# Optimization experiments

Hardware: AMD Instinct MI355X
Metric: run time of the kernel (lower is better)

Reference implementation:

```python
import jax, jax.numpy as jnp
import numpy as np

B, S, D = 8, 512, 768
H, C = 256, 32


def setup_inputs() -> dict:
    key = jax.random.key(0)
    ks = jax.random.split(key, 8)
    scale = 0.05
    return {
        "seq_feats": jax.random.normal(ks[0], (B, S, D), jnp.float32),
        "U": jax.random.normal(ks[1], (H, C, H), jnp.float32) * scale,
        "W_w": jax.random.normal(ks[2], (C, 2 * H), jnp.float32) * scale,
        "W_b": jax.random.normal(ks[3], (C,), jnp.float32) * scale,
        "Ws_w": jax.random.normal(ks[4], (H, D), jnp.float32) * scale,
        "Ws_b": jax.random.normal(ks[5], (H,), jnp.float32) * scale,
        "We_w": jax.random.normal(ks[6], (H, D), jnp.float32) * scale,
        "We_b": jax.random.normal(ks[7], (H,), jnp.float32) * scale,
    }


def reference(seq_feats, U, W_w, W_b, Ws_w, Ws_b, We_w, We_b):
    # start / end projections (torch Linear: x @ W.T + b)
    Hs = seq_feats @ Ws_w.T + Ws_b  # [B,S,H]
    He = seq_feats @ We_w.T + We_b  # [B,S,H]
    # bilinear term: h_s^T U h_e per label
    biaff = jnp.einsum('bsh,hcg,beg->bsec', Hs, U, He)  # [B,S,S,C]
    # concat-linear term rewritten as two broadcast matmuls:
    # W([Hs;He]) = Hs @ W_s.T + He @ W_e.T + b  (identical math, no [B,S,S,2H] intermediate)
    h = Hs.shape[-1]
    W_s, W_e = W_w[:, :h], W_w[:, h:]
    lin = (Hs @ W_s.T)[:, :, None, :] + (He @ W_e.T)[:, None, :, :] + W_b
    return biaff + lin
```

## Files before the change

### kernel.cpp

```cpp
#include <hip/hip_runtime.h>


typedef __bf16 bf16x8 __attribute__((ext_vector_type(8)));
typedef float f32x4 __attribute__((ext_vector_type(4)));
typedef unsigned int u32x4 __attribute__((ext_vector_type(4)));
typedef unsigned int u32x2 __attribute__((ext_vector_type(2)));

union BF8 { unsigned short s[8]; unsigned int u[4]; bf16x8 v; };

__device__ __forceinline__ unsigned short f2bf(float f) {
    unsigned u = __builtin_bit_cast(unsigned, f);
    u += 0x7fffu + ((u >> 16) & 1u);
    return (unsigned short)(u >> 16);
}
__device__ __forceinline__ float bf2f(unsigned short s) {
    unsigned u = ((unsigned)s) << 16;
    return __builtin_bit_cast(float, u);
}
__device__ __forceinline__ bf16x8 load_bf8(const unsigned short* p) {
    return __builtin_bit_cast(bf16x8, *reinterpret_cast<const uint4*>(p));
}
__device__ __forceinline__ ushort4 pack4(float4 v) {
    ushort4 r;
    r.x = f2bf(v.x); r.y = f2bf(v.y); r.z = f2bf(v.z); r.w = f2bf(v.w);
    return r;
}

__global__ __launch_bounds__(256) void kp_conv(
    const float* __restrict__ seq, const float* __restrict__ Ws_w,
    const float* __restrict__ We_w, unsigned short* __restrict__ seqb,
    unsigned short* __restrict__ Wcat) {
    int i = blockIdx.x * 256 + threadIdx.x;
    if (i < 786432) {
        float4 v = ((const float4*)seq)[i];
        ((ushort4*)seqb)[i] = pack4(v);
    } else {
        int j = i - 786432;
        float4 v = (j < 49152) ? ((const float4*)Ws_w)[j]
                               : ((const float4*)We_w)[j - 49152];
        ((ushort4*)Wcat)[j] = pack4(v);
    }
}

__global__ __launch_bounds__(256) void k0_ut(const float* __restrict__ U,
                                             unsigned short* __restrict__ Ut) {
    __shared__ float tile[32][33];
    int tx = threadIdx.x, ty = threadIdx.y;
    int J0 = blockIdx.x * 32, h0 = blockIdx.y * 32;
#pragma unroll
    for (int i = 0; i < 4; i++)
        tile[ty + 8 * i][tx] = U[(h0 + ty + 8 * i) * 8192 + J0 + tx];
    __syncthreads();
#pragma unroll
    for (int i = 0; i < 4; i++)
        Ut[(J0 + ty + 8 * i) * 256 + h0 + tx] = f2bf(tile[tx][ty + 8 * i]);
}

__global__ __launch_bounds__(256) void k1_hs_he(
    const unsigned short* __restrict__ seqb, const unsigned short* __restrict__ Wcat,
    const float* __restrict__ Ws_b, const float* __restrict__ We_b,
    unsigned short* __restrict__ Hs, unsigned short* __restrict__ He) {
    int wid = threadIdx.x >> 6, lane = threadIdx.x & 63;
    int t = lane & 15, q = lane >> 4;
    int wave_id = blockIdx.x * 4 + wid;
    int m0 = (wave_id >> 4) * 32;
    int n0 = (wave_id & 15) * 32;

    const unsigned short* a0 = seqb + (size_t)(m0 + t) * 768;
    const unsigned short* a1 = seqb + (size_t)(m0 + 16 + t) * 768;
    const unsigned short* b0 = Wcat + (size_t)(n0 + t) * 768;
    const unsigned short* b1 = Wcat + (size_t)(n0 + 16 + t) * 768;

    f32x4 acc[2][2];
#pragma unroll
    for (int i = 0; i < 2; i++)
#pragma unroll
        for (int j = 0; j < 2; j++) acc[i][j] = {0.f, 0.f, 0.f, 0.f};

#pragma unroll 4
    for (int kk = 0; kk < 24; kk++) {
        int k = kk * 32 + q * 8;
        bf16x8 af0 = load_bf8(a0 + k);
        bf16x8 af1 = load_bf8(a1 + k);
        bf16x8 bf0 = load_bf8(b0 + k);
        bf16x8 bf1 = load_bf8(b1 + k);
        acc[0][0] = __builtin_amdgcn_mfma_f32_16x16x32_bf16(af0, bf0, acc[0][0], 0, 0, 0);
        acc[0][1] = __builtin_amdgcn_mfma_f32_16x16x32_bf16(af0, bf1, acc[0][1], 0, 0, 0);
        acc[1][0] = __builtin_amdgcn_mfma_f32_16x16x32_bf16(af1, bf0, acc[1][0], 0, 0, 0);
        acc[1][1] = __builtin_amdgcn_mfma_f32_16x16x32_bf16(af1, bf1, acc[1][1], 0, 0, 0);
    }
#pragma unroll
    for (int nt = 0; nt < 2; nt++) {
        int col = n0 + nt * 16 + t;
        float bv;
        unsigned short* dst;
        int c2;
        if (col < 256) { bv = Ws_b[col]; dst = Hs; c2 = col; }
        else           { bv = We_b[col - 256]; dst = He; c2 = col - 256; }
#pragma unroll
        for (int mt = 0; mt < 2; mt++)
#pragma unroll
            for (int r = 0; r < 4; r++) {
                int row = m0 + mt * 16 + q * 4 + r;
                dst[row * 256 + c2] = f2bf(acc[mt][nt][r] + bv);
            }
    }
}

__global__ __launch_bounds__(256) void k2_lin(
    const unsigned short* __restrict__ Hs, const float* __restrict__ W_w,
    const float* __restrict__ W_b, float* __restrict__ linS) {
    int idx = blockIdx.x * 256 + threadIdx.x;
    int c = idx & 31;
    int bs = idx >> 5;
    const unsigned short* Hrow = Hs + bs * 256;
    const float* Wrow = W_w + c * 512;
    float acc = W_b[c];
#pragma unroll 4
    for (int h8 = 0; h8 < 32; h8++) {
        BF8 hv;
        hv.v = load_bf8(Hrow + h8 * 8);
        float4 w0 = *(const float4*)(Wrow + h8 * 8);
        float4 w1 = *(const float4*)(Wrow + h8 * 8 + 4);
        acc += bf2f(hv.s[0]) * w0.x + bf2f(hv.s[1]) * w0.y + bf2f(hv.s[2]) * w0.z +
               bf2f(hv.s[3]) * w0.w + bf2f(hv.s[4]) * w1.x + bf2f(hv.s[5]) * w1.y +
               bf2f(hv.s[6]) * w1.z + bf2f(hv.s[7]) * w1.w;
    }
    linS[bs * 32 + c] = acc;
}

__global__ __launch_bounds__(256) void k3_T(
    const unsigned short* __restrict__ Hs, const unsigned short* __restrict__ Ut,
    const float* __restrict__ W_w, unsigned short* __restrict__ T) {
    int wid = threadIdx.x >> 6, lane = threadIdx.x & 63;
    int t = lane & 15, q = lane >> 4;
    int n_blk = blockIdx.x & 63;
    int mb = (blockIdx.x >> 6) * 4 + wid;
    int c = n_blk >> 1;
    int g0 = (n_blk & 1) * 128;
    int s0 = mb * 32;

    bf16x8 hfr[2][8];
#pragma unroll
    for (int mt = 0; mt < 2; mt++) {
        const unsigned short* arow = Hs + (size_t)(s0 + mt * 16 + t) * 256 + q * 8;
#pragma unroll
        for (int kk = 0; kk < 8; kk++) hfr[mt][kk] = load_bf8(arow + kk * 32);
    }
#pragma unroll 2
    for (int nt = 0; nt < 8; nt++) {
        const unsigned short* grow = Ut + (size_t)(c * 256 + g0 + nt * 16 + t) * 256 + q * 8;
        float4 we = *(const float4*)(W_w + c * 512 + 256 + g0 + nt * 16 + q * 4);
        f32x4 acc0 = {we.x, we.y, we.z, we.w};
        f32x4 acc1 = acc0;
#pragma unroll
        for (int kk = 0; kk < 8; kk++) {
            bf16x8 g = load_bf8(grow + kk * 32);
            acc0 = __builtin_amdgcn_mfma_f32_16x16x32_bf16(g, hfr[0][kk], acc0, 0, 0, 0);
            acc1 = __builtin_amdgcn_mfma_f32_16x16x32_bf16(g, hfr[1][kk], acc1, 0, 0, 0);
        }
        int gidx = g0 + nt * 16 + q * 4;
        u32x2 p0, p1;
        p0.x = (unsigned)f2bf(acc0[0]) | ((unsigned)f2bf(acc0[1]) << 16);
        p0.y = (unsigned)f2bf(acc0[2]) | ((unsigned)f2bf(acc0[3]) << 16);
        p1.x = (unsigned)f2bf(acc1[0]) | ((unsigned)f2bf(acc1[1]) << 16);
        p1.y = (unsigned)f2bf(acc1[2]) | ((unsigned)f2bf(acc1[3]) << 16);
        __builtin_nontemporal_store(p0, (u32x2*)(T + (size_t)((s0 + t) * 32 + c) * 256 + gidx));
        __builtin_nontemporal_store(p1, (u32x2*)(T + (size_t)((s0 + 16 + t) * 32 + c) * 256 + gidx));
    }
}

__global__ __launch_bounds__(256) void k4_out(
    const unsigned short* __restrict__ T, const unsigned short* __restrict__ He,
    const float* __restrict__ linS, float* __restrict__ out) {
    int wid = threadIdx.x >> 6, lane = threadIdx.x & 63;
    int t = lane & 15, q = lane >> 4;
    int b = blockIdx.x & 7;
    int s = (blockIdx.x >> 3) * 4 + wid;
    int bs = b * 512 + s;

    bf16x8 tfr[2][8];
#pragma unroll
    for (int ct = 0; ct < 2; ct++) {
        const unsigned short* brow = T + (size_t)(bs * 32 + ct * 16 + t) * 256 + q * 8;
#pragma unroll
        for (int kk = 0; kk < 8; kk++) {
            u32x4 r = __builtin_nontemporal_load((const u32x4*)(brow + kk * 32));
            tfr[ct][kk] = __builtin_bit_cast(bf16x8, r);
        }
    }
    f32x4 ls0, ls1;
    {
        float4 a = *(const float4*)(linS + bs * 32 + q * 4);
        float4 bv = *(const float4*)(linS + bs * 32 + 16 + q * 4);
        ls0 = {a.x, a.y, a.z, a.w};
        ls1 = {bv.x, bv.y, bv.z, bv.w};
    }
    float* orow = out + (size_t)bs * (512 * 32);
#pragma unroll 2
    for (int e_t = 0; e_t < 32; e_t++) {
        int e0 = e_t * 16;
        const unsigned short* arow = He + (size_t)(b * 512 + e0 + t) * 256 + q * 8;
        f32x4 acc0 = ls0, acc1 = ls1;
#pragma unroll
        for (int kk = 0; kk < 8; kk++) {
            bf16x8 a = load_bf8(arow + kk * 32);
            acc0 = __builtin_amdgcn_mfma_f32_16x16x32_bf16(tfr[0][kk], a, acc0, 0, 0, 0);
            acc1 = __builtin_amdgcn_mfma_f32_16x16x32_bf16(tfr[1][kk], a, acc1, 0, 0, 0);
        }
        float* p = orow + (size_t)(e0 + t) * 32 + q * 4;
        __builtin_nontemporal_store(acc0, (f32x4*)p);
        __builtin_nontemporal_store(acc1, (f32x4*)(p + 16));
    }
}

extern "C" void kernel_launch(void* const* d_in, const int* in_sizes, int n_in,
                              void* d_out, int out_size, void* d_ws, size_t ws_size,
                              hipStream_t stream) {
    const float* seq  = (const float*)d_in[0];
    const float* U    = (const float*)d_in[1];
    const float* W_w  = (const float*)d_in[2];
    const float* W_b  = (const float*)d_in[3];
    const float* Ws_w = (const float*)d_in[4];
    const float* Ws_b = (const float*)d_in[5];
    const float* We_w = (const float*)d_in[6];
    const float* We_b = (const float*)d_in[7];
    float* out = (float*)d_out;

    char* ws = (char*)d_ws;
    unsigned short* Hs   = (unsigned short*)(ws);
    unsigned short* He   = (unsigned short*)(ws + (2ull << 20));
    unsigned short* Ut   = (unsigned short*)(ws + (4ull << 20));
    float* linS          = (float*)(ws + (8ull << 20));
    unsigned short* seqb = (unsigned short*)(ws + (9ull << 20));
    unsigned short* Wcat = (unsigned short*)(ws + (15ull << 20));
    unsigned short* T    = (unsigned short*)(ws + (16ull << 20));

    kp_conv<<<3456, 256, 0, stream>>>(seq, Ws_w, We_w, seqb, Wcat);
    k0_ut<<<dim3(256, 8), dim3(32, 8), 0, stream>>>(U, Ut);
    k1_hs_he<<<512, 256, 0, stream>>>(seqb, Wcat, Ws_b, We_b, Hs, He);
    k2_lin<<<512, 256, 0, stream>>>(Hs, W_w, W_b, linS);
    k3_T<<<2048, 256, 0, stream>>>(Hs, Ut, W_w, T);
    k4_out<<<1024, 256, 0, stream>>>(T, He, linS, out);
}
```

Baseline: 509.2 us.

## Enlarge per-wave register tiles and double-buffer operand loads in k3 and k4

k3_T now covers 64 rows of Hs per wave instead of 32, and k4_out covers two s rows per wave. Each loaded Ut or He fragment therefore feeds twice as many MFMAs, and both grids are halved to match. The next tile's B-operand fragments are prefetched into an alternate register buffer while the current tile's MFMAs run, to hide global load latency. The cost is much higher VGPR use, which may lower occupancy. k4's prefetch also reads one tile past the end of He on the last iteration; the values are never used.

```diff
diff --git a/kernel.cpp b/kernel.cpp
--- a/kernel.cpp
+++ b/kernel.cpp
@@ -138,36 +138,55 @@
     int mb = (blockIdx.x >> 6) * 4 + wid;
     int c = n_blk >> 1;
     int g0 = (n_blk & 1) * 128;
-    int s0 = mb * 32;
-
-    bf16x8 hfr[2][8];
-#pragma unroll
-    for (int mt = 0; mt < 2; mt++) {
+    int s0 = mb * 64;
+
+    bf16x8 hfr[4][8];
+#pragma unroll
+    for (int mt = 0; mt < 4; mt++) {
         const unsigned short* arow = Hs + (size_t)(s0 + mt * 16 + t) * 256 + q * 8;
 #pragma unroll
         for (int kk = 0; kk < 8; kk++) hfr[mt][kk] = load_bf8(arow + kk * 32);
     }
-#pragma unroll 2
-    for (int nt = 0; nt < 8; nt++) {
-        const unsigned short* grow = Ut + (size_t)(c * 256 + g0 + nt * 16 + t) * 256 + q * 8;
-        float4 we = *(const float4*)(W_w + c * 512 + 256 + g0 + nt * 16 + q * 4);
-        f32x4 acc0 = {we.x, we.y, we.z, we.w};
-        f32x4 acc1 = acc0;
-#pragma unroll
-        for (int kk = 0; kk < 8; kk++) {
-            bf16x8 g = load_bf8(grow + kk * 32);
-            acc0 = __builtin_amdgcn_mfma_f32_16x16x32_bf16(g, hfr[0][kk], acc0, 0, 0, 0);
-            acc1 = __builtin_amdgcn_mfma_f32_16x16x32_bf16(g, hfr[1][kk], acc1, 0, 0, 0);
-        }
-        int gidx = g0 + nt * 16 + q * 4;
-        u32x2 p0, p1;
-        p0.x = (unsigned)f2bf(acc0[0]) | ((unsigned)f2bf(acc0[1]) << 16);
-        p0.y = (unsigned)f2bf(acc0[2]) | ((unsigned)f2bf(acc0[3]) << 16);
-        p1.x = (unsigned)f2bf(acc1[0]) | ((unsigned)f2bf(acc1[1]) << 16);
-        p1.y = (unsigned)f2bf(acc1[2]) | ((unsigned)f2bf(acc1[3]) << 16);
-        __builtin_nontemporal_store(p0, (u32x2*)(T + (size_t)((s0 + t) * 32 + c) * 256 + gidx));
-        __builtin_nontemporal_store(p1, (u32x2*)(T + (size_t)((s0 + 16 + t) * 32 + c) * 256 + gidx));
-    }
+
+    const unsigned short* gbase = Ut + (size_t)(c * 256 + g0 + t) * 256 + q * 8;
+    bf16x8 g_cur[8], g_alt[8];
+#pragma unroll
+    for (int kk = 0; kk < 8; kk++) g_cur[kk] = load_bf8(gbase + kk * 32);
+
+#define K3_BODY(NT, GC, GN)                                                      \
+    {                                                                            \
+        const int nt = (NT);                                                     \
+        if (nt + 1 < 8) {                                                        \
+            const unsigned short* gn = gbase + (size_t)(nt + 1) * 16 * 256;      \
+            _Pragma("unroll") for (int kk = 0; kk < 8; kk++)                     \
+                GN[kk] = load_bf8(gn + kk * 32);                                 \
+        }                                                                        \
+        float4 we = *(const float4*)(W_w + c * 512 + 256 + g0 + nt * 16 + q * 4);\
+        f32x4 acc0 = {we.x, we.y, we.z, we.w};                                   \
+        f32x4 acc1 = acc0, acc2 = acc0, acc3 = acc0;                             \
+        _Pragma("unroll") for (int kk = 0; kk < 8; kk++) {                       \
+            acc0 = __builtin_amdgcn_mfma_f32_16x16x32_bf16(GC[kk], hfr[0][kk], acc0, 0, 0, 0); \
+            acc1 = __builtin_amdgcn_mfma_f32_16x16x32_bf16(GC[kk], hfr[1][kk], acc1, 0, 0, 0); \
+            acc2 = __builtin_amdgcn_mfma_f32_16x16x32_bf16(GC[kk], hfr[2][kk], acc2, 0, 0, 0); \
+            acc3 = __builtin_amdgcn_mfma_f32_16x16x32_bf16(GC[kk], hfr[3][kk], acc3, 0, 0, 0); \
+        }                                                                        \
+        int gidx = g0 + nt * 16 + q * 4;                                         \
+        f32x4 av[4] = {acc0, acc1, acc2, acc3};                                  \
+        _Pragma("unroll") for (int m = 0; m < 4; m++) {                          \
+            u32x2 p;                                                             \
+            p.x = (unsigned)f2bf(av[m][0]) | ((unsigned)f2bf(av[m][1]) << 16);   \
+            p.y = (unsigned)f2bf(av[m][2]) | ((unsigned)f2bf(av[m][3]) << 16);   \
+            __builtin_nontemporal_store(                                         \
+                p, (u32x2*)(T + (size_t)((s0 + m * 16 + t) * 32 + c) * 256 + gidx)); \
+        }                                                                        \
+    }
+
+#pragma unroll 1
+    for (int np = 0; np < 4; np++) {
+        K3_BODY(2 * np, g_cur, g_alt)
+        K3_BODY(2 * np + 1, g_alt, g_cur)
+    }
+#undef K3_BODY
 }
 
 __global__ __launch_bounds__(256) void k4_out(
@@ -176,42 +195,64 @@
     int wid = threadIdx.x >> 6, lane = threadIdx.x & 63;
     int t = lane & 15, q = lane >> 4;
     int b = blockIdx.x & 7;
-    int s = (blockIdx.x >> 3) * 4 + wid;
-    int bs = b * 512 + s;
-
-    bf16x8 tfr[2][8];
-#pragma unroll
-    for (int ct = 0; ct < 2; ct++) {
-        const unsigned short* brow = T + (size_t)(bs * 32 + ct * 16 + t) * 256 + q * 8;
-#pragma unroll
-        for (int kk = 0; kk < 8; kk++) {
-            u32x4 r = __builtin_nontemporal_load((const u32x4*)(brow + kk * 32));
-            tfr[ct][kk] = __builtin_bit_cast(bf16x8, r);
+    int s0 = (blockIdx.x >> 3) * 8 + wid * 2;
+    int bs0 = b * 512 + s0;
+
+    bf16x8 tfr[2][2][8];
+#pragma unroll
+    for (int u = 0; u < 2; u++)
+#pragma unroll
+        for (int ct = 0; ct < 2; ct++) {
+            const unsigned short* brow =
+                T + (size_t)((bs0 + u) * 32 + ct * 16 + t) * 256 + q * 8;
+#pragma unroll
+            for (int kk = 0; kk < 8; kk++) {
+                u32x4 r = __builtin_nontemporal_load((const u32x4*)(brow + kk * 32));
+                tfr[u][ct][kk] = __builtin_bit_cast(bf16x8, r);
+            }
         }
-    }
-    f32x4 ls0, ls1;
-    {
-        float4 a = *(const float4*)(linS + bs * 32 + q * 4);
-        float4 bv = *(const float4*)(linS + bs * 32 + 16 + q * 4);
-        ls0 = {a.x, a.y, a.z, a.w};
-        ls1 = {bv.x, bv.y, bv.z, bv.w};
-    }
-    float* orow = out + (size_t)bs * (512 * 32);
-#pragma unroll 2
-    for (int e_t = 0; e_t < 32; e_t++) {
-        int e0 = e_t * 16;
-        const unsigned short* arow = He + (size_t)(b * 512 + e0 + t) * 256 + q * 8;
-        f32x4 acc0 = ls0, acc1 = ls1;
-#pragma unroll
-        for (int kk = 0; kk < 8; kk++) {
-            bf16x8 a = load_bf8(arow + kk * 32);
-            acc0 = __builtin_amdgcn_mfma_f32_16x16x32_bf16(tfr[0][kk], a, acc0, 0, 0, 0);
-            acc1 = __builtin_amdgcn_mfma_f32_16x16x32_bf16(tfr[1][kk], a, acc1, 0, 0, 0);
-        }
-        float* p = orow + (size_t)(e0 + t) * 32 + q * 4;
-        __builtin_nontemporal_store(acc0, (f32x4*)p);
-        __builtin_nontemporal_store(acc1, (f32x4*)(p + 16));
-    }
+    f32x4 ls[2][2];
+#pragma unroll
+    for (int u = 0; u < 2; u++) {
+        float4 a = *(const float4*)(linS + (bs0 + u) * 32 + q * 4);
+        float4 bv = *(const float4*)(linS + (bs0 + u) * 32 + 16 + q * 4);
+        ls[u][0] = {a.x, a.y, a.z, a.w};
+        ls[u][1] = {bv.x, bv.y, bv.z, bv.w};
+    }
+
+    const unsigned short* Hbase = He + (size_t)(b * 512 + t) * 256 + q * 8;
+    bf16x8 a_cur[8], a_alt[8];
+#pragma unroll
+    for (int kk = 0; kk < 8; kk++) a_cur[kk] = load_bf8(Hbase + kk * 32);
+
+#define K4_BODY(ET, AC, AN)                                                      \
+    {                                                                            \
+        const int e_t = (ET);                                                    \
+        const unsigned short* an = Hbase + (size_t)(e_t + 1) * 16 * 256;         \
+        _Pragma("unroll") for (int kk = 0; kk < 8; kk++)                         \
+            AN[kk] = load_bf8(an + kk * 32);                                     \
+        f32x4 acc00 = ls[0][0], acc01 = ls[0][1];                                \
+        f32x4 acc10 = ls[1][0], acc11 = ls[1][1];                                \
+        _Pragma("unroll") for (int kk = 0; kk < 8; kk++) {                       \
+            acc00 = __builtin_amdgcn_mfma_f32_16x16x32_bf16(tfr[0][0][kk], AC[kk], acc00, 0, 0, 0); \
+            acc01 = __builtin_amdgcn_mfma_f32_16x16x32_bf16(tfr[0][1][kk], AC[kk], acc01, 0, 0, 0); \
+            acc10 = __builtin_amdgcn_mfma_f32_16x16x32_bf16(tfr[1][0][kk], AC[kk], acc10, 0, 0, 0); \
+            acc11 = __builtin_amdgcn_mfma_f32_16x16x32_bf16(tfr[1][1][kk], AC[kk], acc11, 0, 0, 0); \
+        }                                                                        \
+        float* p0 = out + (size_t)bs0 * 16384 + (size_t)(e_t * 16 + t) * 32 + q * 4; \
+        __builtin_nontemporal_store(acc00, (f32x4*)p0);                          \
+        __builtin_nontemporal_store(acc01, (f32x4*)(p0 + 16));                   \
+        float* p1 = p0 + 16384;                                                  \
+        __builtin_nontemporal_store(acc10, (f32x4*)p1);                          \
+        __builtin_nontemporal_store(acc11, (f32x4*)(p1 + 16));                   \
+    }
+
+#pragma unroll 1
+    for (int ep = 0; ep < 16; ep++) {
+        K4_BODY(2 * ep, a_cur, a_alt)
+        K4_BODY(2 * ep + 1, a_alt, a_cur)
+    }
+#undef K4_BODY
 }
 
 extern "C" void kernel_launch(void* const* d_in, const int* in_sizes, int n_in,
@@ -240,6 +281,6 @@
     k0_ut<<<dim3(256, 8), dim3(32, 8), 0, stream>>>(U, Ut);
     k1_hs_he<<<512, 256, 0, stream>>>(seqb, Wcat, Ws_b, We_b, Hs, He);
     k2_lin<<<512, 256, 0, stream>>>(Hs, W_w, W_b, linS);
-    k3_T<<<2048, 256, 0, stream>>>(Hs, Ut, W_w, T);
-    k4_out<<<1024, 256, 0, stream>>>(T, He, linS, out);
-}
+    k3_T<<<1024, 256, 0, stream>>>(Hs, Ut, W_w, T);
+    k4_out<<<512, 256, 0, stream>>>(T, He, linS, out);
+}
```

After: 456.8 us, median of 2. 1.11x faster.
